# Performance work log

Hardware: AMD Instinct MI355X
Metric: run time of the kernel (lower is better)

The kernel has to match this reference:

```python
import jax, jax.numpy as jnp
import numpy as np

N_A, N_B, N_C = 100000, 60000, 40000
N = N_A + N_B + N_C  # 200000 total nodes after concat
E = 3200000
D_IN = (512, 256, 128)
D = 64  # com_feat_dim == emb_dim


def setup_inputs() -> dict:
    key = jax.random.key(0)
    ks = jax.random.split(key, 16)
    inp = {
        "feat_a": jax.random.normal(ks[0], (N_A, D_IN[0]), jnp.float32),
        "W_a": jax.random.normal(ks[1], (D_IN[0], D), jnp.float32) * 0.05,
        "b_a": jax.random.normal(ks[2], (D,), jnp.float32) * 0.05,
        "feat_b": jax.random.normal(ks[3], (N_B, D_IN[1]), jnp.float32),
        "W_b": jax.random.normal(ks[4], (D_IN[1], D), jnp.float32) * 0.05,
        "b_b": jax.random.normal(ks[5], (D,), jnp.float32) * 0.05,
        "feat_c": jax.random.normal(ks[6], (N_C, D_IN[2]), jnp.float32),
        "W_c": jax.random.normal(ks[7], (D_IN[2], D), jnp.float32) * 0.05,
        "b_c": jax.random.normal(ks[8], (D,), jnp.float32) * 0.05,
        "gcn_W": jax.random.normal(ks[9], (D, D), jnp.float32) * 0.1,
        "gcn_b": jax.random.normal(ks[10], (D,), jnp.float32) * 0.05,
        "edge_weight": jax.random.uniform(ks[11], (E,), jnp.float32),
        "edge_src": jax.random.randint(ks[12], (E,), 0, N, jnp.int32),
        "edge_dst": jax.random.randint(ks[13], (E,), 0, N, jnp.int32),
    }
    return inp


def reference(feat_a, W_a, b_a, feat_b, W_b, b_b, feat_c, W_c, b_c,
              gcn_W, gcn_b, edge_weight, edge_src, edge_dst):
    # Per-type linear encoders + ReLU, then concat over the node axis
    enc = jnp.concatenate([
        jax.nn.relu(feat_a @ W_a + b_a),
        jax.nn.relu(feat_b @ W_b + b_b),
        jax.nn.relu(feat_c @ W_c + b_c),
    ], axis=0)  # [N, D]
    # GraphConvolution: out = spmm(adj, enc @ W + b)
    support = enc @ gcn_W + gcn_b                    # [N, D]
    msg = support[edge_src] * edge_weight[:, None]   # [E, D] irregular gather
    com_emb = jax.ops.segment_sum(msg, edge_dst, num_segments=N)  # [N, D]
    # F.normalize(p=2, dim=1)
    norm = jnp.linalg.norm(com_emb, axis=1, keepdims=True)
    com_emb = com_emb / jnp.maximum(norm, 1e-12)
    return com_emb
```

## Files before the change

kernel.cpp:

```cpp
#include <hip/hip_runtime.h>

#define N_A 100000
#define N_B 60000
#define N_C 40000
#define NTOT 200000
#define NEDGE 3200000
#define D 64


__device__ __forceinline__ void tile_mm64(const float* __restrict__ sA,
                                          const float* __restrict__ sW,
                                          const int nidx[4], int d0,
                                          float acc[4][2])
{
#pragma unroll
    for (int kk = 0; kk < 64; kk += 4) {
        float wl[4], wh[4];
#pragma unroll
        for (int u = 0; u < 4; ++u) {
            wl[u] = sW[(kk + u) * 64 + d0];
            wh[u] = sW[(kk + u) * 64 + d0 + 32];
        }
#pragma unroll
        for (int j = 0; j < 4; ++j) {
            const float4 f = *(const float4*)(sA + nidx[j] * 64 + kk);
            acc[j][0] = fmaf(f.x, wl[0], acc[j][0]);
            acc[j][0] = fmaf(f.y, wl[1], acc[j][0]);
            acc[j][0] = fmaf(f.z, wl[2], acc[j][0]);
            acc[j][0] = fmaf(f.w, wl[3], acc[j][0]);
            acc[j][1] = fmaf(f.x, wh[0], acc[j][1]);
            acc[j][1] = fmaf(f.y, wh[1], acc[j][1]);
            acc[j][1] = fmaf(f.z, wh[2], acc[j][1]);
            acc[j][1] = fmaf(f.w, wh[3], acc[j][1]);
        }
    }
}

template <int K>
__global__ __launch_bounds__(256) void enc_gcn_kernel(
    const float* __restrict__ feat, const float* __restrict__ W,
    const float* __restrict__ bias, const float* __restrict__ gW,
    const float* __restrict__ gb, float* __restrict__ support, int node0)
{
    __shared__ float sW[64 * 64];
    __shared__ float sF[32 * 64];
    __shared__ float sE[32 * 64];

    const int tid = threadIdx.x;
    const int d0  = tid & 31;
    const int h   = (tid >> 5) & 1;
    const int w   = tid >> 6;
    const int blockNode = blockIdx.x * 32;

    int nidx[4];
#pragma unroll
    for (int j = 0; j < 4; ++j) nidx[j] = j * 8 + w * 2 + h;

    float acc[4][2] = {};

    for (int k0 = 0; k0 < K; k0 += 64) {
#pragma unroll
        for (int i = 0; i < 16; ++i) {
            int idx = i * 256 + tid;
            sW[idx] = W[(long long)(k0 + (idx >> 6)) * 64 + (idx & 63)];
        }
#pragma unroll
        for (int i = 0; i < 8; ++i) {
            int idx = i * 256 + tid;
            sF[idx] = feat[(long long)(blockNode + (idx >> 6)) * K + k0 + (idx & 63)];
        }
        __syncthreads();
        tile_mm64(sF, sW, nidx, d0, acc);
        __syncthreads();
    }

    {
        const float b0 = bias[d0], b1 = bias[d0 + 32];
#pragma unroll
        for (int j = 0; j < 4; ++j) {
            sE[nidx[j] * 64 + d0]      = fmaxf(acc[j][0] + b0, 0.f);
            sE[nidx[j] * 64 + d0 + 32] = fmaxf(acc[j][1] + b1, 0.f);
        }
    }
#pragma unroll
    for (int i = 0; i < 16; ++i) {
        int idx = i * 256 + tid;
        sW[idx] = gW[idx];
    }
    __syncthreads();

    float a2[4][2] = {};
    tile_mm64(sE, sW, nidx, d0, a2);

    const float g0 = gb[d0], g1 = gb[d0 + 32];
#pragma unroll
    for (int j = 0; j < 4; ++j) {
        const long long row = (long long)(node0 + blockNode + nidx[j]);
        support[row * 64 + d0]      = a2[j][0] + g0;
        support[row * 64 + d0 + 32] = a2[j][1] + g1;
    }
}

__global__ void zero_kernel(float4* __restrict__ p, long long n4)
{
    long long i  = (long long)blockIdx.x * blockDim.x + threadIdx.x;
    long long st = (long long)gridDim.x * blockDim.x;
    for (; i < n4; i += st) p[i] = float4{0.f, 0.f, 0.f, 0.f};
}

__global__ void scatter_kernel(const float* __restrict__ support,
                               const float* __restrict__ ew,
                               const int* __restrict__ esrc,
                               const int* __restrict__ edst,
                               float* __restrict__ out, int E)
{
    const int d  = threadIdx.x & 63;
    int gw       = blockIdx.x * (blockDim.x >> 6) + (threadIdx.x >> 6);
    const int nw = gridDim.x * (blockDim.x >> 6);
    for (int e = gw; e < E; e += nw) {
        const int   s = esrc[e];
        const int   t = edst[e];
        const float we = ew[e];
        const float v = support[(long long)s * 64 + d] * we;
        atomicAdd(&out[(long long)t * 64 + d], v);
    }
}

__global__ void normalize_kernel(float* __restrict__ out, int N)
{
    const int d   = threadIdx.x & 63;
    const int row = blockIdx.x * (blockDim.x >> 6) + (threadIdx.x >> 6);
    if (row < N) {
        const long long base = (long long)row * 64;
        float x  = out[base + d];
        float ss = x * x;
#pragma unroll
        for (int o = 32; o; o >>= 1) ss += __shfl_xor(ss, o, 64);
        const float nrm = fmaxf(sqrtf(ss), 1e-12f);
        out[base + d] = x / nrm;
    }
}

extern "C" void kernel_launch(void* const* d_in, const int* in_sizes, int n_in,
                              void* d_out, int out_size, void* d_ws, size_t ws_size,
                              hipStream_t stream)
{
    const float* feat_a = (const float*)d_in[0];
    const float* W_a    = (const float*)d_in[1];
    const float* b_a    = (const float*)d_in[2];
    const float* feat_b = (const float*)d_in[3];
    const float* W_b    = (const float*)d_in[4];
    const float* b_b    = (const float*)d_in[5];
    const float* feat_c = (const float*)d_in[6];
    const float* W_c    = (const float*)d_in[7];
    const float* b_c    = (const float*)d_in[8];
    const float* gcn_W  = (const float*)d_in[9];
    const float* gcn_b  = (const float*)d_in[10];
    const float* ew     = (const float*)d_in[11];
    const int*   esrc   = (const int*)d_in[12];
    const int*   edst   = (const int*)d_in[13];

    float* out     = (float*)d_out;
    float* support = (float*)d_ws;

    zero_kernel<<<2048, 256, 0, stream>>>((float4*)out, (long long)NTOT * D / 4);

    enc_gcn_kernel<512><<<N_A / 32, 256, 0, stream>>>(feat_a, W_a, b_a, gcn_W, gcn_b, support, 0);
    enc_gcn_kernel<256><<<N_B / 32, 256, 0, stream>>>(feat_b, W_b, b_b, gcn_W, gcn_b, support, N_A);
    enc_gcn_kernel<128><<<N_C / 32, 256, 0, stream>>>(feat_c, W_c, b_c, gcn_W, gcn_b, support, N_A + N_B);

    scatter_kernel<<<8192, 256, 0, stream>>>(support, ew, esrc, edst, out, NEDGE);

    normalize_kernel<<<NTOT / 4, 256, 0, stream>>>(out, NTOT);
}
```

Baseline: 1.207 ms.

## Replace atomic edge scatter with per-call CSR build and fused gather-normalize

Builds a destination-sorted CSR on every call: a degree histogram, a three-stage exclusive scan, and an atomic-cursor fill that packs (src, weight) pairs. A per-node gather kernel then sums its incoming messages in registers and applies the L2 normalization in the same kernel. This removes the 64 float atomics per edge into the output and the separate zero and normalize passes. In exchange it adds several small kernels, two integer-atomic passes over the edges, and about 25 MB of CSR writes, and it needs enough workspace or it falls back to the old path.

```diff
diff --git a/kernel.cpp b/kernel.cpp
--- a/kernel.cpp
+++ b/kernel.cpp
@@ -7,6 +7,8 @@
 #define NEDGE 3200000
 #define D 64
 
+#define SCAN_BLK 1024
+#define NB_SCAN ((NTOT + SCAN_BLK - 1) / SCAN_BLK)
 
 __device__ __forceinline__ void tile_mm64(const float* __restrict__ sA,
                                           const float* __restrict__ sW,
@@ -101,6 +103,136 @@
     }
 }
 
+__global__ void zero_ints(int* __restrict__ p, int n)
+{
+    int i = blockIdx.x * blockDim.x + threadIdx.x;
+    if (i < n) p[i] = 0;
+}
+
+__global__ void hist_kernel(const int* __restrict__ edst, int* __restrict__ deg, int e)
+{
+    int i  = blockIdx.x * blockDim.x + threadIdx.x;
+    int st = gridDim.x * blockDim.x;
+    for (; i < e; i += st) atomicAdd(&deg[edst[i]], 1);
+}
+
+__global__ __launch_bounds__(SCAN_BLK) void s1_blocksums(const int* __restrict__ deg,
+                                                         int* __restrict__ partials, int n)
+{
+    const int tid = threadIdx.x;
+    const int i   = blockIdx.x * SCAN_BLK + tid;
+    int v = (i < n) ? deg[i] : 0;
+#pragma unroll
+    for (int o = 32; o; o >>= 1) v += __shfl_xor(v, o, 64);
+    __shared__ int wsum[SCAN_BLK / 64];
+    if ((tid & 63) == 0) wsum[tid >> 6] = v;
+    __syncthreads();
+    if (tid == 0) {
+        int s = 0;
+#pragma unroll
+        for (int w = 0; w < SCAN_BLK / 64; ++w) s += wsum[w];
+        partials[blockIdx.x] = s;
+    }
+}
+
+__global__ __launch_bounds__(256) void s2_scan(const int* __restrict__ partials,
+                                               int* __restrict__ pscan, int np)
+{
+    __shared__ int arr[512];
+    if (threadIdx.x < np) arr[threadIdx.x] = partials[threadIdx.x];
+    __syncthreads();
+    if (threadIdx.x == 0) {
+        int run = 0;
+        for (int i = 0; i < np; ++i) { int t = arr[i]; arr[i] = run; run += t; }
+    }
+    __syncthreads();
+    if (threadIdx.x < np) pscan[threadIdx.x] = arr[threadIdx.x];
+}
+
+__global__ __launch_bounds__(SCAN_BLK) void s3_scan(const int* __restrict__ deg,
+                                                    const int* __restrict__ pscan,
+                                                    int* __restrict__ row_start,
+                                                    int* __restrict__ cursor, int n)
+{
+    const int tid  = threadIdx.x;
+    const int lane = tid & 63, wid = tid >> 6;
+    const int i    = blockIdx.x * SCAN_BLK + tid;
+    int v = (i < n) ? deg[i] : 0;
+    int x = v;
+#pragma unroll
+    for (int o = 1; o < 64; o <<= 1) {
+        int y = __shfl_up(x, o, 64);
+        if (lane >= o) x += y;
+    }
+    __shared__ int wsum[SCAN_BLK / 64];
+    if (lane == 63) wsum[wid] = x;
+    __syncthreads();
+    if (tid == 0) {
+        int run = 0;
+#pragma unroll
+        for (int w = 0; w < SCAN_BLK / 64; ++w) { int t = wsum[w]; wsum[w] = run; run += t; }
+    }
+    __syncthreads();
+    if (i < n) {
+        const int excl = x - v + wsum[wid] + pscan[blockIdx.x];
+        row_start[i] = excl;
+        cursor[i]    = excl;
+    }
+}
+
+__global__ void fill_kernel(const int* __restrict__ esrc, const int* __restrict__ edst,
+                            const float* __restrict__ ew, int* __restrict__ cursor,
+                            uint2* __restrict__ csr, int e)
+{
+    int i  = blockIdx.x * blockDim.x + threadIdx.x;
+    int st = gridDim.x * blockDim.x;
+    for (; i < e; i += st) {
+        const int t   = edst[i];
+        const int pos = atomicAdd(&cursor[t], 1);
+        csr[pos] = make_uint2((unsigned)esrc[i], __float_as_uint(ew[i]));
+    }
+}
+
+__global__ __launch_bounds__(256) void gather_norm_kernel(const float* __restrict__ support,
+                                                          const uint2* __restrict__ csr,
+                                                          const int* __restrict__ row_start,
+                                                          const int* __restrict__ deg,
+                                                          float* __restrict__ out)
+{
+    const int lane = threadIdx.x & 63;
+    const int nid  = blockIdx.x * 4 + (threadIdx.x >> 6);
+    if (nid >= NTOT) return;
+    const int base = row_start[nid];
+    const int dg   = deg[nid];
+
+    float acc = 0.f;
+    int i = 0;
+    for (; i + 4 <= dg; i += 4) {
+        const uint2 c0 = csr[base + i + 0];
+        const uint2 c1 = csr[base + i + 1];
+        const uint2 c2 = csr[base + i + 2];
+        const uint2 c3 = csr[base + i + 3];
+        const float v0 = support[(long long)c0.x * D + lane];
+        const float v1 = support[(long long)c1.x * D + lane];
+        const float v2 = support[(long long)c2.x * D + lane];
+        const float v3 = support[(long long)c3.x * D + lane];
+        acc = fmaf(v0, __uint_as_float(c0.y), acc);
+        acc = fmaf(v1, __uint_as_float(c1.y), acc);
+        acc = fmaf(v2, __uint_as_float(c2.y), acc);
+        acc = fmaf(v3, __uint_as_float(c3.y), acc);
+    }
+    for (; i < dg; ++i) {
+        const uint2 c = csr[base + i];
+        acc = fmaf(support[(long long)c.x * D + lane], __uint_as_float(c.y), acc);
+    }
+
+    float ss = acc * acc;
+#pragma unroll
+    for (int o = 32; o; o >>= 1) ss += __shfl_xor(ss, o, 64);
+    const float nrm = fmaxf(sqrtf(ss), 1e-12f);
+    out[(long long)nid * D + lane] = acc / nrm;
+}
+
 __global__ void zero_kernel(float4* __restrict__ p, long long n4)
 {
     long long i  = (long long)blockIdx.x * blockDim.x + threadIdx.x;
@@ -118,11 +250,10 @@
     int gw       = blockIdx.x * (blockDim.x >> 6) + (threadIdx.x >> 6);
     const int nw = gridDim.x * (blockDim.x >> 6);
     for (int e = gw; e < E; e += nw) {
-        const int   s = esrc[e];
-        const int   t = edst[e];
+        const int   s  = esrc[e];
+        const int   t  = edst[e];
         const float we = ew[e];
-        const float v = support[(long long)s * 64 + d] * we;
-        atomicAdd(&out[(long long)t * 64 + d], v);
+        atomicAdd(&out[(long long)t * 64 + d], support[(long long)s * 64 + d] * we);
     }
 }
 
@@ -160,16 +291,43 @@
     const int*   esrc   = (const int*)d_in[12];
     const int*   edst   = (const int*)d_in[13];
 
-    float* out     = (float*)d_out;
-    float* support = (float*)d_ws;
-
-    zero_kernel<<<2048, 256, 0, stream>>>((float4*)out, (long long)NTOT * D / 4);
+    float* out = (float*)d_out;
+
+    char* ws = (char*)d_ws;
+    const size_t off_support = 0;
+    const size_t off_deg     = off_support + (size_t)NTOT * D * 4;
+    const size_t off_rowst   = off_deg   + (size_t)NTOT * 4;
+    const size_t off_cursor  = off_rowst + (size_t)NTOT * 4;
+    const size_t off_part    = off_cursor + (size_t)NTOT * 4;
+    const size_t off_pscan   = off_part  + 1024;
+    const size_t off_csr     = off_pscan + 1024;
+    const size_t need        = off_csr + (size_t)NEDGE * 8;
+
+    float* support = (float*)(ws + off_support);
 
     enc_gcn_kernel<512><<<N_A / 32, 256, 0, stream>>>(feat_a, W_a, b_a, gcn_W, gcn_b, support, 0);
     enc_gcn_kernel<256><<<N_B / 32, 256, 0, stream>>>(feat_b, W_b, b_b, gcn_W, gcn_b, support, N_A);
     enc_gcn_kernel<128><<<N_C / 32, 256, 0, stream>>>(feat_c, W_c, b_c, gcn_W, gcn_b, support, N_A + N_B);
 
-    scatter_kernel<<<8192, 256, 0, stream>>>(support, ew, esrc, edst, out, NEDGE);
-
-    normalize_kernel<<<NTOT / 4, 256, 0, stream>>>(out, NTOT);
-}
+    if (ws_size >= need) {
+        int*   deg     = (int*)(ws + off_deg);
+        int*   rowst   = (int*)(ws + off_rowst);
+        int*   cursor  = (int*)(ws + off_cursor);
+        int*   part    = (int*)(ws + off_part);
+        int*   pscan   = (int*)(ws + off_pscan);
+        uint2* csr     = (uint2*)(ws + off_csr);
+
+        zero_ints<<<(NTOT + 255) / 256, 256, 0, stream>>>(deg, NTOT);
+        hist_kernel<<<4096, 256, 0, stream>>>(edst, deg, NEDGE);
+        s1_blocksums<<<NB_SCAN, SCAN_BLK, 0, stream>>>(deg, part, NTOT);
+        s2_scan<<<1, 256, 0, stream>>>(part, pscan, NB_SCAN);
+        s3_scan<<<NB_SCAN, SCAN_BLK, 0, stream>>>(deg, pscan, rowst, cursor, NTOT);
+        fill_kernel<<<4096, 256, 0, stream>>>(esrc, edst, ew, cursor, csr, NEDGE);
+
+        gather_norm_kernel<<<(NTOT + 3) / 4, 256, 0, stream>>>(support, csr, rowst, deg, out);
+    } else {
+        zero_kernel<<<2048, 256, 0, stream>>>((float4*)out, (long long)NTOT * D / 4);
+        scatter_kernel<<<8192, 256, 0, stream>>>(support, ew, esrc, edst, out, NEDGE);
+        normalize_kernel<<<NTOT / 4, 256, 0, stream>>>(out, NTOT);
+    }
+}
```

New measurement: 1.042 ms. 13.6% less time.
